# Kernel optimization log

Hardware: AMD Instinct MI355X
Metric: run time of the kernel (lower is better)

## Reference

```python
import jax, jax.numpy as jnp
import numpy as np

B, T, N, D = 2, 4, 4096, 64
DEG = 16
G = B * T                 # number of periodic structures
NNODE = G * N             # total atoms
E = NNODE * DEG           # total edges
EPS_LEN = 1e-12


def setup_inputs() -> dict:
    key = jax.random.key(0)
    ks = jax.random.split(key, 16)
    x = jax.random.normal(ks[0], (B, T, N, 3), jnp.float32) * 3.0
    x1 = jax.random.normal(ks[1], (B, T, N, 3), jnp.float32) * 3.0
    t = jax.random.uniform(ks[2], (B,), jnp.float32)
    # near-orthorhombic lattices, box size ~20 A
    cell = jnp.eye(3, dtype=jnp.float32)[None, None] * 20.0 \
        + 0.1 * jax.random.normal(ks[3], (B, T, 3, 3), jnp.float32)
    v_mask = (jax.random.uniform(ks[4], (B, T, N, 1)) > 0.1).astype(jnp.float32)
    # edges: both endpoints within the same structure's node block
    eps = E // G  # edges per structure
    local = jax.random.randint(ks[5], (2, E), 0, N, jnp.int32)
    offs = (jnp.repeat(jnp.arange(G, dtype=jnp.int32), eps) * N)[None, :]
    edge_index = local + offs
    to_jimages = jax.random.randint(ks[6], (E, 3), 0, 3, jnp.int32) - 1  # {-1,0,1}
    s = 1.0 / np.sqrt(D)
    return {
        "x": x, "t": t, "cell": cell, "x1": x1, "v_mask": v_mask,
        "W_species": jax.random.normal(ks[7], (5, D), jnp.float32) * s,
        "W_t": jax.random.normal(ks[8], (1, D), jnp.float32) * s,
        "W_edge": jax.random.normal(ks[9], (4, D), jnp.float32) * s,
        "W_msg": jax.random.normal(ks[10], (3 * D, D), jnp.float32) * s,
        "W_upd": jax.random.normal(ks[11], (D, D), jnp.float32) * s,
        "w_dec": jax.random.normal(ks[12], (D,), jnp.float32) * s,
        "edge_index": edge_index,
        "to_jimages": to_jimages,
    }


def reference(x, t, cell, x1, v_mask, W_species, W_t, W_edge, W_msg, W_upd,
              w_dec, edge_index, to_jimages):
    b, tt, n_at, _ = x.shape
    n = b * tt * n_at
    # forward(): x = x * v_mask + x1 * (1 - v_mask)  (potential_model=False)
    pos = (x * v_mask + x1 * (1.0 - v_mask)).reshape(n, 3)
    cells = cell.reshape(-1, 3, 3)                       # [G,3,3]
    src, dst = edge_index[0], edge_index[1]
    edge_graph = src // n_at                              # structure id per edge
    # get_pbc_distances: offsets = to_jimages @ cell  (per-edge gather)
    offsets = jnp.einsum('ek,ekl->el', to_jimages.astype(pos.dtype),
                         cells[edge_graph])               # [E,3]
    edge_vec = pos[dst] - pos[src] + offsets              # [E,3]
    edge_len = jnp.sqrt(jnp.sum(edge_vec * edge_vec, -1, keepdims=True) + EPS_LEN)
    edge_attr = jnp.concatenate([edge_vec, edge_len], -1)  # hstack -> [E,4]
    # per-node time feature [n,1]
    t_node = jnp.broadcast_to(t[:, None, None, None], (b, tt, n_at, 1)).reshape(n, 1)
    # species = one_hot(zeros, 5) -> [n,5]
    species = jnp.zeros((n, 5), x.dtype).at[:, 0].set(1.0)
    # encoder: scalar embedding from species + time; edge embedding; v starts at 0
    h = species @ W_species + t_node @ W_t                # [n,D]
    ea = jax.nn.silu(edge_attr @ W_edge)                  # [E,D]
    # processor: one equivariant message-passing step
    msg = jax.nn.silu(jnp.concatenate([h[src], h[dst], ea], -1) @ W_msg)  # [E,D]
    agg = jax.ops.segment_sum(msg, dst, num_segments=n)   # [n,D]
    h = h + jax.nn.silu(agg @ W_upd)
    mv = edge_vec[:, :, None] * msg[:, None, :]           # [E,3,D] vector messages
    v = jax.ops.segment_sum(mv.reshape(-1, 3 * mv.shape[-1]), dst,
                            num_segments=n).reshape(n, 3, -1)  # [n,3,D]
    # decoder: gated equivariant readout -> per-atom 3-vector
    vec_out = jnp.einsum('ncd,d->nc', v * jax.nn.silu(h)[:, None, :], w_dec)
    out = vec_out.reshape(b, tt, n_at, 3) * v_mask
    return out
```

## Files before the change

### kernel.cpp

```cpp
#include <hip/hip_runtime.h>
#include <math.h>

#define NNODE 32768
#define NEDGE 524288
#define DD 64

typedef float  f32x4 __attribute__((ext_vector_type(4)));
typedef short  s16x8 __attribute__((ext_vector_type(8)));

__device__ __forceinline__ float silu_f(float x) {
    return x * __builtin_amdgcn_rcpf(1.0f + __expf(-x));
}
__device__ __forceinline__ unsigned cvt_pk_bf16(float a, float b) {
    unsigned r;
    asm("v_cvt_pk_bf16_f32 %0, %1, %2" : "=v"(r) : "v"(a), "v"(b));
    return r;
}
__device__ __forceinline__ unsigned short bf16r(float f) {
    unsigned u = __float_as_uint(f);
    unsigned r = (u + 0x7FFFu + ((u >> 16) & 1u)) >> 16;
    return (unsigned short)r;
}
__device__ __forceinline__ float bf16f(unsigned short u) {
    return __uint_as_float(((unsigned)u) << 16);
}
__device__ __forceinline__ void wsync() {
    asm volatile("s_waitcnt lgkmcnt(0)" ::: "memory");
    __builtin_amdgcn_sched_barrier(0);
}

__global__ __launch_bounds__(256) void k_prep_hist_base(
    const float* __restrict__ x, const float* __restrict__ x1,
    const float* __restrict__ vm, float* __restrict__ pos,
    const int* __restrict__ ei, int* __restrict__ cnt, int* __restrict__ rank,
    const float* __restrict__ Wsp, const float* __restrict__ Wt,
    const float* __restrict__ Wm, const float* __restrict__ Wu,
    const float* __restrict__ We, const float* __restrict__ tarr,
    float* __restrict__ base_ws, unsigned short* __restrict__ wfrag)
{
    int tid = threadIdx.x, b = blockIdx.x;
    if (b >= 2048) {
        if (b < 2056) {
            #pragma unroll
            for (int j = 0; j < 5; ++j) {
                int idx = (b - 2048) * 1280 + j * 256 + tid;
                unsigned short v;
                if (idx < 8192) {
                    int sel = idx >> 12, id2 = idx & 4095;
                    int jj = id2 & 7;
                    int ln = (id2 >> 3) & 63;
                    int ts = id2 >> 9;
                    int t2 = ts >> 1, s = ts & 1;
                    int k   = s*32 + (ln >> 4)*8 + jj;
                    int col = t2*16 + (ln & 15);
                    v = bf16r(sel ? Wu[k*DD + col] : Wm[(128 + k)*DD + col]);
                } else {
                    int id3 = idx - 8192;
                    int jj = id3 & 7, ln = (id3 >> 3) & 63, t2 = id3 >> 9;
                    v = (ln < 16 && jj < 4) ? bf16r(We[jj*DD + t2*16 + (ln & 15)])
                                            : (unsigned short)0;
                }
                wfrag[idx] = v;
            }
        } else if (tid < 64) {
            float t0 = tarr[0], t1 = tarr[1];
            float aA = 0.0f, aB = 0.0f;
            #pragma unroll 8
            for (int k = 0; k < DD; ++k) {
                float w = Wm[k*DD + tid] + Wm[(DD+k)*DD + tid];
                aA = fmaf(Wsp[k] + t0*Wt[k], w, aA);
                aB = fmaf(Wsp[k] + t1*Wt[k], w, aB);
            }
            base_ws[tid]      = aA;
            base_ws[DD + tid] = aB;
        }
        return;
    }
    if (b < 128) {
        int i = b*256 + tid;
        float m = vm[i];
        #pragma unroll
        for (int c = 0; c < 3; ++c)
            pos[i*3+c] = x[i*3+c]*m + x1[i*3+c]*(1.0f-m);
    }
    int e = (b & 7) * 65536 + (b >> 3) * 256 + tid;
    rank[e] = atomicAdd(&cnt[ei[NEDGE + e]], 1);
}

__global__ __launch_bounds__(1024) void k_scan(
    const int* __restrict__ cnt, int* __restrict__ rowptr)
{
    __shared__ int buf[2][1024];
    const int g = blockIdx.x;
    const int tid = threadIdx.x;
    int4 L = ((const int4*)cnt)[g*1024 + tid];
    int s = L.x + L.y + L.z + L.w;
    buf[0][tid] = s;
    __syncthreads();
    int pp = 0;
    for (int off = 1; off < 1024; off <<= 1) {
        int v = buf[pp][tid];
        if (tid >= off) v += buf[pp][tid - off];
        buf[pp^1][tid] = v;
        __syncthreads();
        pp ^= 1;
    }
    int ex = (tid ? buf[pp][tid-1] : 0) + g*65536;
    int4 o;
    o.x = ex; ex += L.x;
    o.y = ex; ex += L.y;
    o.z = ex; ex += L.z;
    o.w = ex; ex += L.w;
    ((int4*)rowptr)[g*1024 + tid] = o;
    if (g == 7 && tid == 1023) rowptr[32768] = NEDGE;
}

__global__ __launch_bounds__(256) void k_sortgeo(
    const int* __restrict__ ei, const int* __restrict__ tj,
    const float* __restrict__ pos, const float* __restrict__ cell,
    const int* __restrict__ rowptr, const int* __restrict__ rank,
    float4* __restrict__ srec, int* __restrict__ sdst)
{
    int b = blockIdx.x;
    int e = (b & 7) * 65536 + (b >> 3) * 256 + threadIdx.x;
    int g = b & 7;
    int src = ei[e];
    int dst = ei[NEDGE + e];
    const float* cl = cell + g*9;
    float c00=cl[0],c01=cl[1],c02=cl[2],c10=cl[3],c11=cl[4],c12=cl[5],c20=cl[6],c21=cl[7],c22=cl[8];
    float tj0 = (float)tj[e*3+0], tj1 = (float)tj[e*3+1], tj2 = (float)tj[e*3+2];
    float ev0 = pos[dst*3+0] - pos[src*3+0] + tj0*c00 + tj1*c10 + tj2*c20;
    float ev1 = pos[dst*3+1] - pos[src*3+1] + tj0*c01 + tj1*c11 + tj2*c21;
    float ev2 = pos[dst*3+2] - pos[src*3+2] + tj0*c02 + tj1*c12 + tj2*c22;
    float len = sqrtf(ev0*ev0 + ev1*ev1 + ev2*ev2 + 1e-12f);
    int slot = rowptr[dst] + rank[e];
    srec[slot] = (float4){ev0, ev1, ev2, len};
    sdst[slot] = dst;
}

__global__ __launch_bounds__(64) void k_edge_all(
    const float4* __restrict__ srec, const int* __restrict__ sdst,
    const int* __restrict__ rowptr,
    const unsigned short* __restrict__ wfrag,
    const float* __restrict__ base_ws,
    const float* __restrict__ Wsp, const float* __restrict__ Wt,
    const float* __restrict__ wdec, const float* __restrict__ tarr,
    const float* __restrict__ vm, float* __restrict__ out)
{
    const int lane = threadIdx.x;
    const int lo16 = lane & 15;
    const int hi   = lane >> 4;
    const int grp  = (blockIdx.x & 7) * 1024 + (blockIdx.x >> 3);
    const int n0   = grp * 4;

    __shared__ __align__(16) char my[8320];
    float4*         edge4 = (float4*)my;
    int*            dstl  = (int*)(my + 1024);
    unsigned short* ealds = (unsigned short*)(my + 1280);
    unsigned short* msgb  = (unsigned short*)(my + 3584);
    unsigned short* agg_l = (unsigned short*)(my + 6144);
    unsigned short* v_l   = (unsigned short*)(my + 6720);

    {
        int* zp = (int*)(my + 6144);
        #pragma unroll
        for (int j = 0; j < 9; ++j) {
            int o = j*64 + lane;
            if (o < 528) zp[o] = 0;
        }
    }

    s16x8 bfr[4][2], wfe[4];
    #pragma unroll
    for (int t2 = 0; t2 < 4; ++t2) {
        #pragma unroll
        for (int s = 0; s < 2; ++s)
            bfr[t2][s] = *(const s16x8*)(wfrag + ((t2*2+s)*64 + lane)*8);
        wfe[t2] = *(const s16x8*)(wfrag + 8192 + (t2*64 + lane)*8);
    }
    const bool  sb  = (n0 >> 14) != 0;
    float bv4[4];
    #pragma unroll
    for (int t2 = 0; t2 < 4; ++t2)
        bv4[t2] = base_ws[(sb ? DD : 0) + t2*16 + lo16];

    const int estart = rowptr[n0];
    const int eend   = rowptr[n0 + 4];

    int   curn = -1, lastdst = -1;
    float s0 = 0.f, sva = 0.f, svb = 0.f, svc = 0.f;

    int ebase = estart;
    int cnt64 = eend - ebase; if (cnt64 > 64) cnt64 = 64;
    float4 r_rec = {0.f,0.f,0.f,0.f};
    int    r_dst = 0;
    if (ebase < eend) {
        int ii = ebase + (lane < cnt64 ? lane : cnt64 - 1);
        r_rec = srec[ii];
        r_dst = sdst[ii];
    }

    while (ebase < eend) {
        edge4[lane] = r_rec;
        dstl[lane]  = r_dst;
        wsync();

        int prev = __shfl_up(r_dst, 1, 64);
        if (lane == 0) prev = lastdst;
        unsigned long long bmask = __ballot(r_dst != prev);
        lastdst = __shfl(r_dst, 63, 64);

        int nb = ebase + 64;
        if (nb < eend) {
            int c2 = eend - nb; if (c2 > 64) c2 = 64;
            int jj = nb + (lane < c2 ? lane : c2 - 1);
            r_rec = srec[jj];
            r_dst = sdst[jj];
        }

        int nsub = (cnt64 + 15) >> 4;
        for (int i = 0; i < nsub; ++i) {
            float4 q = edge4[i*16 + lo16];
            unsigned pa0 = cvt_pk_bf16(q.x, q.y);
            unsigned pa1 = cvt_pk_bf16(q.z, q.w);
            uint4 av = (hi == 0) ? (uint4){pa0, pa1, 0u, 0u}
                                 : (uint4){0u, 0u, 0u, 0u};
            s16x8 aea = *reinterpret_cast<s16x8*>(&av);
            #pragma unroll
            for (int t2 = 0; t2 < 4; ++t2) {
                f32x4 pre = {0.f, 0.f, 0.f, 0.f};
                pre = __builtin_amdgcn_mfma_f32_16x16x32_bf16(aea, wfe[t2], pre, 0, 0, 0);
                #pragma unroll
                for (int r = 0; r < 4; ++r)
                    ealds[(hi*4+r)*72 + t2*16 + lo16] =
                        (unsigned short)cvt_pk_bf16(silu_f(pre[r]), 0.f);
            }
            wsync();

            const unsigned short* arow = ealds + lo16*72 + hi*8;
            s16x8 a0 = *(const s16x8*)(arow);
            s16x8 a1 = *(const s16x8*)(arow + 32);

            #pragma unroll
            for (int t2 = 0; t2 < 4; ++t2) {
                const float bvt = bv4[t2];
                f32x4 acc = {bvt, bvt, bvt, bvt};
                acc = __builtin_amdgcn_mfma_f32_16x16x32_bf16(a0, bfr[t2][0], acc, 0, 0, 0);
                acc = __builtin_amdgcn_mfma_f32_16x16x32_bf16(a1, bfr[t2][1], acc, 0, 0, 0);
                unsigned u0 = cvt_pk_bf16(silu_f(acc[0]), silu_f(acc[1]));
                unsigned u1 = cvt_pk_bf16(silu_f(acc[2]), silu_f(acc[3]));
                *reinterpret_cast<uint2*>(msgb + (t2*16+lo16)*20 + hi*4) = (uint2){u0, u1};
            }
            wsync();

            int rows = cnt64 - i*16; if (rows > 16) rows = 16;
            #pragma unroll
            for (int rb = 0; rb < 4; ++rb) {
                if (rb*4 < rows) {
                    uint2 mm = *reinterpret_cast<const uint2*>(msgb + lane*20 + rb*4);
                    float m0 = __uint_as_float(mm.x << 16);
                    float m1 = __uint_as_float(mm.x & 0xffff0000u);
                    float m2 = __uint_as_float(mm.y << 16);
                    float m3 = __uint_as_float(mm.y & 0xffff0000u);
                    #pragma unroll
                    for (int rr = 0; rr < 4; ++rr) {
                        int rl = rb*4 + rr;
                        if (rl < rows) {
                            if ((bmask >> (i*16 + rl)) & 1) {
                                if (curn >= 0) {
                                    int nl = curn - n0;
                                    agg_l[nl*72 + lane]     = (unsigned short)cvt_pk_bf16(s0, s0);
                                    v_l[(nl*3+0)*64 + lane] = (unsigned short)cvt_pk_bf16(sva, sva);
                                    v_l[(nl*3+1)*64 + lane] = (unsigned short)cvt_pk_bf16(svb, svb);
                                    v_l[(nl*3+2)*64 + lane] = (unsigned short)cvt_pk_bf16(svc, svc);
                                }
                                s0 = sva = svb = svc = 0.f;
                                curn = dstl[i*16 + rl];
                            }
                            float4 q2 = edge4[i*16 + rl];
                            float m = rr==0 ? m0 : rr==1 ? m1 : rr==2 ? m2 : m3;
                            s0 += m;
                            sva = fmaf(q2.x, m, sva);
                            svb = fmaf(q2.y, m, svb);
                            svc = fmaf(q2.z, m, svc);
                        }
                    }
                }
            }
        }
        ebase = nb;
        cnt64 = eend - ebase; if (cnt64 > 64) cnt64 = 64;
    }
    if (curn >= 0) {
        int nl = curn - n0;
        agg_l[nl*72 + lane]     = (unsigned short)cvt_pk_bf16(s0, s0);
        v_l[(nl*3+0)*64 + lane] = (unsigned short)cvt_pk_bf16(sva, sva);
        v_l[(nl*3+1)*64 + lane] = (unsigned short)cvt_pk_bf16(svb, svb);
        v_l[(nl*3+2)*64 + lane] = (unsigned short)cvt_pk_bf16(svc, svc);
    }
    wsync();

    s16x8 wub[4][2];
    #pragma unroll
    for (int t2 = 0; t2 < 4; ++t2)
        #pragma unroll
        for (int s = 0; s < 2; ++s)
            wub[t2][s] = *(const s16x8*)(wfrag + 4096 + ((t2*2+s)*64 + lane)*8);
    const float tb = sb ? tarr[1] : tarr[0];
    float hb4[4], wd4[4];
    #pragma unroll
    for (int t2 = 0; t2 < 4; ++t2) {
        hb4[t2] = Wsp[t2*16+lo16] + tb * Wt[t2*16+lo16];
        wd4[t2] = wdec[t2*16+lo16];
    }
    s16x8 ga0 = *(const s16x8*)(agg_l + lo16*72 + hi*8);
    s16x8 ga1 = *(const s16x8*)(agg_l + lo16*72 + hi*8 + 32);
    float p[4][3] = {{0.f,0.f,0.f},{0.f,0.f,0.f},{0.f,0.f,0.f},{0.f,0.f,0.f}};
    #pragma unroll
    for (int t2 = 0; t2 < 4; ++t2) {
        f32x4 accg = {0.f, 0.f, 0.f, 0.f};
        accg = __builtin_amdgcn_mfma_f32_16x16x32_bf16(ga0, wub[t2][0], accg, 0, 0, 0);
        accg = __builtin_amdgcn_mfma_f32_16x16x32_bf16(ga1, wub[t2][1], accg, 0, 0, 0);
        #pragma unroll
        for (int r = 0; r < 4; ++r) {
            int node = hi*4 + r;
            float hn   = hb4[t2] + silu_f(accg[r]);
            float gate = silu_f(hn) * wd4[t2];
            if (node < 4) {
                #pragma unroll
                for (int c = 0; c < 3; ++c) {
                    float vv = bf16f(v_l[(node*3+c)*64 + t2*16 + lo16]);
                    p[r][c] = fmaf(gate, vv, p[r][c]);
                }
            }
        }
    }
    #pragma unroll
    for (int st = 1; st < 16; st <<= 1)
        #pragma unroll
        for (int r = 0; r < 4; ++r)
            #pragma unroll
            for (int c = 0; c < 3; ++c)
                p[r][c] += __shfl_xor(p[r][c], st, 64);

    if (lo16 < 12 && hi == 0) {
        int rr = lo16 / 3, c = lo16 - rr*3;
        float val = rr==0 ? (c==0 ? p[0][0] : c==1 ? p[0][1] : p[0][2])
                  : rr==1 ? (c==0 ? p[1][0] : c==1 ? p[1][1] : p[1][2])
                  : rr==2 ? (c==0 ? p[2][0] : c==1 ? p[2][1] : p[2][2])
                  :         (c==0 ? p[3][0] : c==1 ? p[3][1] : p[3][2]);
        out[(n0 + rr)*3 + c] = val * vm[n0 + rr];
    }
}

extern "C" void kernel_launch(void* const* d_in, const int* in_sizes, int n_in,
                              void* d_out, int out_size, void* d_ws, size_t ws_size,
                              hipStream_t stream) {
    const float* x    = (const float*)d_in[0];
    const float* t    = (const float*)d_in[1];
    const float* cell = (const float*)d_in[2];
    const float* x1   = (const float*)d_in[3];
    const float* vm   = (const float*)d_in[4];
    const float* Wsp  = (const float*)d_in[5];
    const float* Wt   = (const float*)d_in[6];
    const float* We   = (const float*)d_in[7];
    const float* Wm   = (const float*)d_in[8];
    const float* Wu   = (const float*)d_in[9];
    const float* wdec = (const float*)d_in[10];
    const int*   ei   = (const int*)d_in[11];
    const int*   tj   = (const int*)d_in[12];
    float* out = (float*)d_out;

    float*  ws      = (float*)d_ws;
    float4* srec    = (float4*)ws;
    int*    sdst    = (int*)(ws + 2097152);
    float*  pos     = ws + 2621440;
    int*    rank    = (int*)(pos + 98304);
    int*    rowptr  = rank + 524288;
    int*    cnt     = rowptr + 32784;
    float*  base_ws = (float*)(cnt + 32768);
    unsigned short* wfrag = (unsigned short*)(base_ws + 128);

    hipMemsetAsync(cnt, 0, 32768*sizeof(int), stream);
    k_prep_hist_base<<<2057, 256, 0, stream>>>(x, x1, vm, pos, ei, cnt, rank,
                                               Wsp, Wt, Wm, Wu, We, t, base_ws, wfrag);
    k_scan<<<8, 1024, 0, stream>>>(cnt, rowptr);
    k_sortgeo<<<2048, 256, 0, stream>>>(ei, tj, pos, cell, rowptr, rank, srec, sdst);
    k_edge_all<<<8192, 64, 0, stream>>>(srec, sdst, rowptr, wfrag, base_ws,
                                        Wsp, Wt, wdec, t, vm, out);
}
```

Before: 87.35 us.

## Pad per-node edge segments to multiples of four and accumulate with LDS atomics

The scan now builds a second row-pointer array whose per-node edge counts are rounded up to multiples of four. Each group of four MFMA rows therefore belongs to a single destination node, so the serial per-row segmented reduction and the stored dst array are replaced by a 4-row partial sum followed by LDS float atomics into fp32 aggregates. Padding rows are zero records; their constant silu(base) contribution is subtracted from the scalar aggregate afterwards. In exchange it adds a memset of the padded edge buffer, a second scan, and some extra padded MFMA work.

```diff
diff --git a/kernel.cpp b/kernel.cpp
--- a/kernel.cpp
+++ b/kernel.cpp
@@ -4,6 +4,9 @@
 #define NNODE 32768
 #define NEDGE 524288
 #define DD 64
+#define E4CAP 622592
+#define SSTRIDE 77824
+#define RP4S 4100
 
 typedef float  f32x4 __attribute__((ext_vector_type(4)));
 typedef short  s16x8 __attribute__((ext_vector_type(8)));
@@ -20,9 +23,6 @@
     unsigned u = __float_as_uint(f);
     unsigned r = (u + 0x7FFFu + ((u >> 16) & 1u)) >> 16;
     return (unsigned short)r;
-}
-__device__ __forceinline__ float bf16f(unsigned short u) {
-    return __uint_as_float(((unsigned)u) << 16);
 }
 __device__ __forceinline__ void wsync() {
     asm volatile("s_waitcnt lgkmcnt(0)" ::: "memory");
@@ -88,7 +88,7 @@
 }
 
 __global__ __launch_bounds__(1024) void k_scan(
-    const int* __restrict__ cnt, int* __restrict__ rowptr)
+    const int* __restrict__ cnt, int* __restrict__ rowptr, int* __restrict__ rowptr4)
 {
     __shared__ int buf[2][1024];
     const int g = blockIdx.x;
@@ -113,13 +113,34 @@
     o.w = ex; ex += L.w;
     ((int4*)rowptr)[g*1024 + tid] = o;
     if (g == 7 && tid == 1023) rowptr[32768] = NEDGE;
+    __syncthreads();
+    int4 P = { (L.x+3)&~3, (L.y+3)&~3, (L.z+3)&~3, (L.w+3)&~3 };
+    int s4 = P.x + P.y + P.z + P.w;
+    buf[0][tid] = s4;
+    __syncthreads();
+    pp = 0;
+    for (int off = 1; off < 1024; off <<= 1) {
+        int v = buf[pp][tid];
+        if (tid >= off) v += buf[pp][tid - off];
+        buf[pp^1][tid] = v;
+        __syncthreads();
+        pp ^= 1;
+    }
+    int ex4 = (tid ? buf[pp][tid-1] : 0) + g*SSTRIDE;
+    int4 o4;
+    o4.x = ex4; ex4 += P.x;
+    o4.y = ex4; ex4 += P.y;
+    o4.z = ex4; ex4 += P.z;
+    o4.w = ex4; ex4 += P.w;
+    *(int4*)(rowptr4 + g*RP4S + tid*4) = o4;
+    if (tid == 1023) rowptr4[g*RP4S + 4096] = ex4;
 }
 
 __global__ __launch_bounds__(256) void k_sortgeo(
     const int* __restrict__ ei, const int* __restrict__ tj,
     const float* __restrict__ pos, const float* __restrict__ cell,
-    const int* __restrict__ rowptr, const int* __restrict__ rank,
-    float4* __restrict__ srec, int* __restrict__ sdst)
+    const int* __restrict__ rowptr4, const int* __restrict__ rank,
+    float4* __restrict__ srec4)
 {
     int b = blockIdx.x;
     int e = (b & 7) * 65536 + (b >> 3) * 256 + threadIdx.x;
@@ -133,14 +154,13 @@
     float ev1 = pos[dst*3+1] - pos[src*3+1] + tj0*c01 + tj1*c11 + tj2*c21;
     float ev2 = pos[dst*3+2] - pos[src*3+2] + tj0*c02 + tj1*c12 + tj2*c22;
     float len = sqrtf(ev0*ev0 + ev1*ev1 + ev2*ev2 + 1e-12f);
-    int slot = rowptr[dst] + rank[e];
-    srec[slot] = (float4){ev0, ev1, ev2, len};
-    sdst[slot] = dst;
+    int slot = rowptr4[g*RP4S + (dst & 4095)] + rank[e];
+    srec4[slot] = (float4){ev0, ev1, ev2, len};
 }
 
 __global__ __launch_bounds__(64) void k_edge_all(
-    const float4* __restrict__ srec, const int* __restrict__ sdst,
-    const int* __restrict__ rowptr,
+    const float4* __restrict__ srec4,
+    const int* __restrict__ rowptr, const int* __restrict__ rowptr4,
     const unsigned short* __restrict__ wfrag,
     const float* __restrict__ base_ws,
     const float* __restrict__ Wsp, const float* __restrict__ Wt,
@@ -153,20 +173,18 @@
     const int grp  = (blockIdx.x & 7) * 1024 + (blockIdx.x >> 3);
     const int n0   = grp * 4;
 
-    __shared__ __align__(16) char my[8320];
+    __shared__ __align__(16) char my[8768];
     float4*         edge4 = (float4*)my;
-    int*            dstl  = (int*)(my + 1024);
-    unsigned short* ealds = (unsigned short*)(my + 1280);
-    unsigned short* msgb  = (unsigned short*)(my + 3584);
-    unsigned short* agg_l = (unsigned short*)(my + 6144);
-    unsigned short* v_l   = (unsigned short*)(my + 6720);
+    unsigned short* ealds = (unsigned short*)(my + 1024);
+    float*          aggf  = (float*)(my + 3328);
+    float*          vf    = (float*)(my + 4688);
 
     {
-        int* zp = (int*)(my + 6144);
-        #pragma unroll
-        for (int j = 0; j < 9; ++j) {
+        int* zp = (int*)(my + 3328);
+        #pragma unroll
+        for (int j = 0; j < 22; ++j) {
             int o = j*64 + lane;
-            if (o < 528) zp[o] = 0;
+            if (o < 1360) zp[o] = 0;
         }
     }
 
@@ -183,39 +201,41 @@
     #pragma unroll
     for (int t2 = 0; t2 < 4; ++t2)
         bv4[t2] = base_ws[(sb ? DD : 0) + t2*16 + lo16];
-
-    const int estart = rowptr[n0];
-    const int eend   = rowptr[n0 + 4];
-
-    int   curn = -1, lastdst = -1;
-    float s0 = 0.f, sva = 0.f, svb = 0.f, svc = 0.f;
+    const float sbase = silu_f(base_ws[(sb ? DD : 0) + lane]);
+
+    const int gS = n0 >> 12;
+    const int li = gS*RP4S + (n0 & 4095);
+    int rp4a[5], npad[4];
+    #pragma unroll
+    for (int k = 0; k <= 4; ++k)
+        rp4a[k] = __builtin_amdgcn_readfirstlane(rowptr4[li + k]);
+    #pragma unroll
+    for (int k = 0; k < 4; ++k) {
+        int r0 = __builtin_amdgcn_readfirstlane(rowptr[n0 + k]);
+        int r1 = __builtin_amdgcn_readfirstlane(rowptr[n0 + k + 1]);
+        npad[k] = (rp4a[k+1] - rp4a[k]) - (r1 - r0);
+    }
+
+    const int estart = rp4a[0];
+    const int eend   = rp4a[4];
 
     int ebase = estart;
     int cnt64 = eend - ebase; if (cnt64 > 64) cnt64 = 64;
     float4 r_rec = {0.f,0.f,0.f,0.f};
-    int    r_dst = 0;
     if (ebase < eend) {
         int ii = ebase + (lane < cnt64 ? lane : cnt64 - 1);
-        r_rec = srec[ii];
-        r_dst = sdst[ii];
+        r_rec = srec4[ii];
     }
 
     while (ebase < eend) {
         edge4[lane] = r_rec;
-        dstl[lane]  = r_dst;
         wsync();
-
-        int prev = __shfl_up(r_dst, 1, 64);
-        if (lane == 0) prev = lastdst;
-        unsigned long long bmask = __ballot(r_dst != prev);
-        lastdst = __shfl(r_dst, 63, 64);
 
         int nb = ebase + 64;
         if (nb < eend) {
             int c2 = eend - nb; if (c2 > 64) c2 = 64;
             int jj = nb + (lane < c2 ? lane : c2 - 1);
-            r_rec = srec[jj];
-            r_dst = sdst[jj];
+            r_rec = srec4[jj];
         }
 
         int nsub = (cnt64 + 15) >> 4;
@@ -241,62 +261,39 @@
             s16x8 a0 = *(const s16x8*)(arow);
             s16x8 a1 = *(const s16x8*)(arow + 32);
 
+            float4 e0 = edge4[i*16 + hi*4 + 0];
+            float4 e1 = edge4[i*16 + hi*4 + 1];
+            float4 e2 = edge4[i*16 + hi*4 + 2];
+            float4 e3 = edge4[i*16 + hi*4 + 3];
+            const int sc = ebase + i*16 + (hi << 2);
+            int nl = (sc >= rp4a[1]) + (sc >= rp4a[2]) + (sc >= rp4a[3]) + (sc >= rp4a[4]);
+            float* ag = aggf + nl*68;
+            float* vg = vf + nl*204;
+
             #pragma unroll
             for (int t2 = 0; t2 < 4; ++t2) {
                 const float bvt = bv4[t2];
                 f32x4 acc = {bvt, bvt, bvt, bvt};
                 acc = __builtin_amdgcn_mfma_f32_16x16x32_bf16(a0, bfr[t2][0], acc, 0, 0, 0);
                 acc = __builtin_amdgcn_mfma_f32_16x16x32_bf16(a1, bfr[t2][1], acc, 0, 0, 0);
-                unsigned u0 = cvt_pk_bf16(silu_f(acc[0]), silu_f(acc[1]));
-                unsigned u1 = cvt_pk_bf16(silu_f(acc[2]), silu_f(acc[3]));
-                *reinterpret_cast<uint2*>(msgb + (t2*16+lo16)*20 + hi*4) = (uint2){u0, u1};
-            }
-            wsync();
-
-            int rows = cnt64 - i*16; if (rows > 16) rows = 16;
-            #pragma unroll
-            for (int rb = 0; rb < 4; ++rb) {
-                if (rb*4 < rows) {
-                    uint2 mm = *reinterpret_cast<const uint2*>(msgb + lane*20 + rb*4);
-                    float m0 = __uint_as_float(mm.x << 16);
-                    float m1 = __uint_as_float(mm.x & 0xffff0000u);
-                    float m2 = __uint_as_float(mm.y << 16);
-                    float m3 = __uint_as_float(mm.y & 0xffff0000u);
-                    #pragma unroll
-                    for (int rr = 0; rr < 4; ++rr) {
-                        int rl = rb*4 + rr;
-                        if (rl < rows) {
-                            if ((bmask >> (i*16 + rl)) & 1) {
-                                if (curn >= 0) {
-                                    int nl = curn - n0;
-                                    agg_l[nl*72 + lane]     = (unsigned short)cvt_pk_bf16(s0, s0);
-                                    v_l[(nl*3+0)*64 + lane] = (unsigned short)cvt_pk_bf16(sva, sva);
-                                    v_l[(nl*3+1)*64 + lane] = (unsigned short)cvt_pk_bf16(svb, svb);
-                                    v_l[(nl*3+2)*64 + lane] = (unsigned short)cvt_pk_bf16(svc, svc);
-                                }
-                                s0 = sva = svb = svc = 0.f;
-                                curn = dstl[i*16 + rl];
-                            }
-                            float4 q2 = edge4[i*16 + rl];
-                            float m = rr==0 ? m0 : rr==1 ? m1 : rr==2 ? m2 : m3;
-                            s0 += m;
-                            sva = fmaf(q2.x, m, sva);
-                            svb = fmaf(q2.y, m, svb);
-                            svc = fmaf(q2.z, m, svc);
-                        }
-                    }
-                }
+                float m0 = silu_f(acc[0]), m1 = silu_f(acc[1]);
+                float m2 = silu_f(acc[2]), m3 = silu_f(acc[3]);
+                const int ch = t2*16 + lo16;
+                atomicAdd(&ag[ch],      (m0+m1)+(m2+m3));
+                atomicAdd(&vg[ch],      fmaf(e0.x,m0, fmaf(e1.x,m1, fmaf(e2.x,m2, e3.x*m3))));
+                atomicAdd(&vg[68+ch],   fmaf(e0.y,m0, fmaf(e1.y,m1, fmaf(e2.y,m2, e3.y*m3))));
+                atomicAdd(&vg[136+ch],  fmaf(e0.z,m0, fmaf(e1.z,m1, fmaf(e2.z,m2, e3.z*m3))));
             }
         }
         ebase = nb;
         cnt64 = eend - ebase; if (cnt64 > 64) cnt64 = 64;
     }
-    if (curn >= 0) {
-        int nl = curn - n0;
-        agg_l[nl*72 + lane]     = (unsigned short)cvt_pk_bf16(s0, s0);
-        v_l[(nl*3+0)*64 + lane] = (unsigned short)cvt_pk_bf16(sva, sva);
-        v_l[(nl*3+1)*64 + lane] = (unsigned short)cvt_pk_bf16(svb, svb);
-        v_l[(nl*3+2)*64 + lane] = (unsigned short)cvt_pk_bf16(svc, svc);
+    wsync();
+
+    #pragma unroll
+    for (int k = 0; k < 4; ++k) {
+        float a = aggf[k*68 + lane] - (float)npad[k] * sbase;
+        ealds[k*72 + lane] = (unsigned short)cvt_pk_bf16(a, a);
     }
     wsync();
 
@@ -313,8 +310,8 @@
         hb4[t2] = Wsp[t2*16+lo16] + tb * Wt[t2*16+lo16];
         wd4[t2] = wdec[t2*16+lo16];
     }
-    s16x8 ga0 = *(const s16x8*)(agg_l + lo16*72 + hi*8);
-    s16x8 ga1 = *(const s16x8*)(agg_l + lo16*72 + hi*8 + 32);
+    s16x8 ga0 = *(const s16x8*)(ealds + lo16*72 + hi*8);
+    s16x8 ga1 = *(const s16x8*)(ealds + lo16*72 + hi*8 + 32);
     float p[4][3] = {{0.f,0.f,0.f},{0.f,0.f,0.f},{0.f,0.f,0.f},{0.f,0.f,0.f}};
     #pragma unroll
     for (int t2 = 0; t2 < 4; ++t2) {
@@ -328,10 +325,8 @@
             float gate = silu_f(hn) * wd4[t2];
             if (node < 4) {
                 #pragma unroll
-                for (int c = 0; c < 3; ++c) {
-                    float vv = bf16f(v_l[(node*3+c)*64 + t2*16 + lo16]);
-                    p[r][c] = fmaf(gate, vv, p[r][c]);
-                }
+                for (int c = 0; c < 3; ++c)
+                    p[r][c] = fmaf(gate, vf[(node*3+c)*68 + t2*16 + lo16], p[r][c]);
             }
         }
     }
@@ -372,20 +367,21 @@
     float* out = (float*)d_out;
 
     float*  ws      = (float*)d_ws;
-    float4* srec    = (float4*)ws;
-    int*    sdst    = (int*)(ws + 2097152);
-    float*  pos     = ws + 2621440;
+    float4* srec4   = (float4*)ws;
+    float*  pos     = ws + 2490368;
     int*    rank    = (int*)(pos + 98304);
     int*    rowptr  = rank + 524288;
-    int*    cnt     = rowptr + 32784;
+    int*    rowptr4 = rowptr + 32772;
+    int*    cnt     = rowptr4 + 32800;
     float*  base_ws = (float*)(cnt + 32768);
     unsigned short* wfrag = (unsigned short*)(base_ws + 128);
 
     hipMemsetAsync(cnt, 0, 32768*sizeof(int), stream);
+    hipMemsetAsync(srec4, 0, (size_t)E4CAP*16, stream);
     k_prep_hist_base<<<2057, 256, 0, stream>>>(x, x1, vm, pos, ei, cnt, rank,
                                                Wsp, Wt, Wm, Wu, We, t, base_ws, wfrag);
-    k_scan<<<8, 1024, 0, stream>>>(cnt, rowptr);
-    k_sortgeo<<<2048, 256, 0, stream>>>(ei, tj, pos, cell, rowptr, rank, srec, sdst);
-    k_edge_all<<<8192, 64, 0, stream>>>(srec, sdst, rowptr, wfrag, base_ws,
+    k_scan<<<8, 1024, 0, stream>>>(cnt, rowptr, rowptr4);
+    k_sortgeo<<<2048, 256, 0, stream>>>(ei, tj, pos, cell, rowptr4, rank, srec4);
+    k_edge_all<<<8192, 64, 0, stream>>>(srec4, rowptr, rowptr4, wfrag, base_ws,
                                         Wsp, Wt, wdec, t, vm, out);
 }
```

Result: slower. 277.4 us (+217.6%).
